# Kernel optimization log

Hardware: AMD Instinct MI355X
Metric: run time of the kernel (lower is better)

## Reference

```python
import jax, jax.numpy as jnp
import numpy as np

DIM_MODEL = 1024
NUM_HEADS = 16
HEAD_DIM = DIM_MODEL // NUM_HEADS


def setup_inputs() -> dict:
    key = jax.random.key(0)
    ks = jax.random.split(key, 10)
    B, S1, S2, D = 2, 1, 2048, DIM_MODEL
    q = jax.random.normal(ks[0], (B, S1, S2, 1, D), dtype=jnp.float32)
    k = jax.random.normal(ks[1], (B, S1, S2, 1, D), dtype=jnp.float32)
    v = jax.random.normal(ks[2], (B, S1, S2, 1, D), dtype=jnp.float32)
    mask = jnp.zeros((1,), dtype=jnp.bool_)
    inv_scale_factor = jnp.ones((1, 1, 1, 1), dtype=jnp.float32)
    s = 1.0 / np.sqrt(D)
    Wq = jax.random.uniform(ks[3], (D, D), jnp.float32, -s, s)
    bq = jax.random.uniform(ks[4], (D,), jnp.float32, -s, s)
    Wk = jax.random.uniform(ks[5], (D, D), jnp.float32, -s, s)
    bk = jax.random.uniform(ks[6], (D,), jnp.float32, -s, s)
    Wv = jax.random.uniform(ks[7], (D, D), jnp.float32, -s, s)
    bv = jax.random.uniform(ks[8], (D,), jnp.float32, -s, s)
    return {"q": q, "k": k, "v": v, "mask": mask, "inv_scale_factor": inv_scale_factor,
            "Wq": Wq, "bq": bq, "Wk": Wk, "bk": bk, "Wv": Wv, "bv": bv}


def reference(q, k, v, mask, inv_scale_factor, Wq, bq, Wk, bk, Wv, bv):
    # q,k,v: [B, S1, S2, 1, D]; mask is unused (faithful to source forward)
    B, S1, S2, _, D = q.shape
    H, Dh = NUM_HEADS, HEAD_DIM

    def proj(x, W, b):
        # torch Linear: x @ W.T + b, then view -> heads, transpose(2,3)
        y = jnp.einsum('bgsod,ed->bgsoe', x, W) + b  # o==1 collapses in reshape
        return jnp.swapaxes(y.reshape(B, S1, S2, H, Dh), 2, 3)  # [B,S1,H,S2,Dh]

    qh = proj(q, Wq, bq) / jnp.sqrt(jnp.asarray(Dh, q.dtype))
    kh = proj(k, Wk, bk)
    vh = proj(v, Wv, bv)

    scores = jnp.einsum('bghsd,bghtd->bghst', qh, kh) / inv_scale_factor  # [B,S1,H,S2,S2]
    p = jax.nn.softmax(scores.astype(jnp.float32), axis=-1).astype(q.dtype)
    # dropout_p=0 (eval): identity
    out = jnp.einsum('bghst,bghtd->bghsd', p, vh)  # [B,S1,H,S2,Dh]
    out = out.reshape(B, S1, H, S2 * Dh)
    out = jnp.transpose(out, (0, 1, 3, 2))  # torch transpose(2,3)
    return out.reshape(B, S1, -1)
```

## Files before the change

### kernel.cpp

```cpp
#include <hip/hip_runtime.h>
#include <stdint.h>

typedef short bf16x8 __attribute__((ext_vector_type(8)));
typedef float f32x4 __attribute__((ext_vector_type(4)));

static __device__ __forceinline__ unsigned short f2bf(float f) {
  union { float f; uint32_t u; } c; c.f = f;
  uint32_t u = c.u;
  uint32_t r = (u + 0x7fffu + ((u >> 16) & 1u)) >> 16;
  return (unsigned short)r;
}

extern "C" __device__ float __ocml_exp2_f32(float);
static __device__ __forceinline__ float exp2_(float x) {
#if __has_builtin(__builtin_amdgcn_exp2f)
  return __builtin_amdgcn_exp2f(x);
#else
  return __ocml_exp2_f32(x);
#endif
}

static __device__ __forceinline__ uint32_t cvtpk_bf16(float a, float b) {
  uint32_t r;
  asm("v_cvt_pk_bf16_f32 %0, %1, %2" : "=v"(r) : "v"(a), "v"(b));
  return r;
}

__device__ __forceinline__ void gload_lds16(const void* g, void* l) {
  __builtin_amdgcn_global_load_lds((const __attribute__((address_space(1))) uint32_t*)g,
                                   (__attribute__((address_space(3))) uint32_t*)l, 16, 0, 0);
}

__global__ __launch_bounds__(256) void k_convert(
    const float* __restrict__ q, const float* __restrict__ k, const float* __restrict__ v,
    const float* __restrict__ Wq, const float* __restrict__ Wk, const float* __restrict__ Wv,
    unsigned short* __restrict__ Xb, unsigned short* __restrict__ Wb) {
  const int NX4 = 3145728;
  const int NW4 = 786432;
  int i = blockIdx.x * 256 + threadIdx.x;
  if (i >= NX4 + NW4) return;
  const float* src; unsigned short* dst; int off4;
  if (i < NX4) {
    int a = i >> 20; off4 = i & 1048575;
    src = (a == 0) ? q : (a == 1) ? k : v;
    dst = Xb + (size_t)a * 4194304;
  } else {
    int j = i - NX4;
    int a = j >> 18; off4 = j & 262143;
    src = (a == 0) ? Wq : (a == 1) ? Wk : Wv;
    dst = Wb + (size_t)a * 1048576;
  }
  float4 f = ((const float4*)src)[off4];
  uint32_t lo = (uint32_t)f2bf(f.x) | ((uint32_t)f2bf(f.y) << 16);
  uint32_t hi = (uint32_t)f2bf(f.z) | ((uint32_t)f2bf(f.w) << 16);
  ((uint2*)dst)[off4] = make_uint2(lo, hi);
}

__global__ __launch_bounds__(256) void k_proj(
    const unsigned short* __restrict__ Xb, const unsigned short* __restrict__ Wb,
    const float* __restrict__ bq, const float* __restrict__ bk, const float* __restrict__ bv,
    const float* __restrict__ inv_scale,
    unsigned short* __restrict__ Qh, unsigned short* __restrict__ Kh,
    unsigned short* __restrict__ VhT) {
  __shared__ __align__(16) unsigned short At[128 * 32];
  __shared__ __align__(16) unsigned short Bt[128 * 32];
  const int g = blockIdx.y;
  const int m0 = (blockIdx.x & 31) * 128, n0 = (blockIdx.x >> 5) * 128;
  const unsigned short* X = Xb + (size_t)g * 4194304;
  const unsigned short* W = Wb + (size_t)g * 1048576;
  const int tid = threadIdx.x;
  const int w = tid >> 6, lane = tid & 63;
  const int wr = w >> 1, wc = w & 1;
  const int lq = lane & 15, lg = lane >> 4;

  f32x4 acc[4][4];
#pragma unroll
  for (int a = 0; a < 4; a++)
#pragma unroll
    for (int b = 0; b < 4; b++) acc[a][b] = (f32x4){0.f, 0.f, 0.f, 0.f};

  for (int kt = 0; kt < 32; ++kt) {
#pragma unroll
    for (int p = 0; p < 2; ++p) {
      int i = (w * 2 + p) * 64 + lane;
      int row = i >> 2, c = i & 3;
      gload_lds16(X + (size_t)(m0 + row) * 1024 + kt * 32 + c * 8, (char*)At + i * 16);
      gload_lds16(W + (size_t)(n0 + row) * 1024 + kt * 32 + c * 8, (char*)Bt + i * 16);
    }
    __syncthreads();
    bf16x8 af[4], bfr[4];
#pragma unroll
    for (int mi = 0; mi < 4; mi++)
      af[mi] = *(const bf16x8*)((const char*)At + ((wr * 64 + mi * 16 + lq) * 64 + lg * 16));
#pragma unroll
    for (int ni = 0; ni < 4; ni++)
      bfr[ni] = *(const bf16x8*)((const char*)Bt + ((wc * 64 + ni * 16 + lq) * 64 + lg * 16));
#pragma unroll
    for (int mi = 0; mi < 4; mi++)
#pragma unroll
      for (int ni = 0; ni < 4; ni++)
        acc[mi][ni] = __builtin_amdgcn_mfma_f32_16x16x32_bf16(af[mi], bfr[ni], acc[mi][ni], 0, 0, 0);
    __syncthreads();
  }

  const float* bias = (g == 0) ? bq : (g == 1) ? bk : bv;
  const float scale = (g == 0) ? 0.125f * 1.4426950408889634f / inv_scale[0] : 1.0f;
#pragma unroll
  for (int ni = 0; ni < 4; ni++) {
    int col = n0 + wc * 64 + ni * 16 + lq;
    float bb = bias[col];
    int h = col >> 6, dh = col & 63;
#pragma unroll
    for (int mi = 0; mi < 4; mi++) {
#pragma unroll
      for (int r = 0; r < 4; r++) {
        int row = m0 + wr * 64 + mi * 16 + lg * 4 + r;
        int b = row >> 11, s2 = row & 2047;
        unsigned short bv16 = f2bf((acc[mi][ni][r] + bb) * scale);
        if (g == 0)
          Qh[(size_t)(b * 16 + h) * 131072 + (size_t)s2 * 64 + dh] = bv16;
        else if (g == 1)
          Kh[(size_t)(b * 16 + h) * 131072 + (size_t)s2 * 64 + dh] = bv16;
        else
          VhT[(size_t)((b * 16 + h) * 64 + dh) * 2048 + s2] = bv16;
      }
    }
  }
}

__global__ __launch_bounds__(256, 2) void k_attn(
    const unsigned short* __restrict__ Qh, const unsigned short* __restrict__ Kh,
    const unsigned short* __restrict__ VhT, float* __restrict__ Ot) {
  __shared__ __align__(16) unsigned short Kt[3][64 * 64];
  __shared__ __align__(16) unsigned short Vt[3][64 * 64];
  __shared__ __align__(16) unsigned short Pl[4][32][64];
  const int n = blockIdx.x;
  const int xcd = n & 7, slot = n >> 3;
  const int bh = (xcd << 2) | (slot >> 4);
  const int qt = slot & 15;
  const int tid = threadIdx.x;
  const int w = tid >> 6, lane = tid & 63;
  const int lq = lane & 15, lg = lane >> 4;
  const int qbase = qt * 128 + w * 32;

  bf16x8 qf[2][2];
#pragma unroll
  for (int r = 0; r < 2; r++) {
    const unsigned short* qp = Qh + ((size_t)bh * 2048 + qbase + r * 16 + lq) * 64 + lg * 8;
    qf[r][0] = *(const bf16x8*)(qp);
    qf[r][1] = *(const bf16x8*)(qp + 32);
  }

  f32x4 ofr[4][2];
#pragma unroll
  for (int dt = 0; dt < 4; dt++)
#pragma unroll
    for (int r = 0; r < 2; r++) ofr[dt][r] = (f32x4){0.f, 0.f, 0.f, 0.f};
  float m[2] = {-INFINITY, -INFINITY}, l[2] = {0.f, 0.f};

  const unsigned short* kgbase = Kh + (size_t)bh * 131072;
  const unsigned short* vgbase = VhT + (size_t)bh * 131072;

  auto STAGE = [&](int tile, int buf) {
#pragma unroll
    for (int p = 0; p < 2; ++p) {
      int i = p * 256 + tid;
      int row = i >> 3, c = i & 7;
      int cs = c ^ (row & 7);
      gload_lds16(kgbase + (size_t)(tile * 64 + row) * 64 + cs * 8, (char*)Kt[buf] + i * 16);
      gload_lds16(vgbase + (size_t)row * 2048 + tile * 64 + cs * 8, (char*)Vt[buf] + i * 16);
    }
  };

  STAGE(0, 0);
  STAGE(1, 1);

  for (int kv = 0; kv < 32; ++kv) {
    if (kv == 31) {
      asm volatile("s_waitcnt vmcnt(0)" ::: "memory");
    } else {
      asm volatile("s_waitcnt vmcnt(4)" ::: "memory");
    }
    __builtin_amdgcn_s_barrier();
    __builtin_amdgcn_sched_barrier(0);

    if (kv < 30) STAGE(kv + 2, (kv + 2) % 3);

    const char* ktc = (const char*)Kt[kv % 3];
    const char* vtc = (const char*)Vt[kv % 3];

    f32x4 sf[4][2];
#pragma unroll
    for (int t4 = 0; t4 < 4; t4++) {
      int row = t4 * 16 + lq;
      int c0 = lg ^ (row & 7), c1 = (4 + lg) ^ (row & 7);
      bf16x8 ka = *(const bf16x8*)(ktc + row * 128 + c0 * 16);
      bf16x8 kc = *(const bf16x8*)(ktc + row * 128 + c1 * 16);
#pragma unroll
      for (int r = 0; r < 2; r++) {
        f32x4 z = (f32x4){0.f, 0.f, 0.f, 0.f};
        z = __builtin_amdgcn_mfma_f32_16x16x32_bf16(ka, qf[r][0], z, 0, 0, 0);
        z = __builtin_amdgcn_mfma_f32_16x16x32_bf16(kc, qf[r][1], z, 0, 0, 0);
        sf[t4][r] = z;
      }
    }

    float pmax[2];
#pragma unroll
    for (int r = 0; r < 2; r++) {
      float a0 = fmaxf(fmaxf(sf[0][r][0], sf[0][r][1]), fmaxf(sf[0][r][2], sf[0][r][3]));
      float a1 = fmaxf(fmaxf(sf[1][r][0], sf[1][r][1]), fmaxf(sf[1][r][2], sf[1][r][3]));
      float a2 = fmaxf(fmaxf(sf[2][r][0], sf[2][r][1]), fmaxf(sf[2][r][2], sf[2][r][3]));
      float a3 = fmaxf(fmaxf(sf[3][r][0], sf[3][r][1]), fmaxf(sf[3][r][2], sf[3][r][3]));
      float a = fmaxf(fmaxf(a0, a1), fmaxf(a2, a3));
      a = fmaxf(a, __shfl_xor(a, 16));
      a = fmaxf(a, __shfl_xor(a, 32));
      pmax[r] = a;
    }
    if (__any((pmax[0] > m[0] + 8.f) || (pmax[1] > m[1] + 8.f))) {
#pragma unroll
      for (int r = 0; r < 2; r++) {
        float mn = fmaxf(m[r], pmax[r]);
        float c = exp2_(m[r] - mn);
        m[r] = mn;
        l[r] *= c;
#pragma unroll
        for (int dt = 0; dt < 4; dt++) ofr[dt][r] *= c;
      }
    }

#pragma unroll
    for (int r = 0; r < 2; r++) {
      float ps = 0.f;
#pragma unroll
      for (int t4 = 0; t4 < 4; t4++) {
        float p0 = exp2_(sf[t4][r][0] - m[r]);
        float p1 = exp2_(sf[t4][r][1] - m[r]);
        float p2 = exp2_(sf[t4][r][2] - m[r]);
        float p3 = exp2_(sf[t4][r][3] - m[r]);
        ps += (p0 + p1) + (p2 + p3);
        uint32_t w0 = cvtpk_bf16(p0, p1);
        uint32_t w1 = cvtpk_bf16(p2, p3);
        uint64_t dw = (uint64_t)w0 | ((uint64_t)w1 << 32);
        int ch = (t4 * 2 + (lg >> 1)) ^ (lq & 7);
        __builtin_memcpy((char*)&Pl[w][r * 16 + lq][0] + ch * 16 + (lg & 1) * 8, &dw, 8);
      }
      ps += __shfl_xor(ps, 16);
      ps += __shfl_xor(ps, 32);
      l[r] += ps;
    }

    bf16x8 pf[2][2];
#pragma unroll
    for (int r = 0; r < 2; r++)
#pragma unroll
      for (int c = 0; c < 2; c++) {
        int ch = (c * 4 + lg) ^ (lq & 7);
        __builtin_memcpy(&pf[r][c], (const char*)&Pl[w][r * 16 + lq][0] + ch * 16, 16);
      }
    __builtin_amdgcn_s_setprio(1);
#pragma unroll
    for (int dt = 0; dt < 4; dt++) {
      int row = dt * 16 + lq;
      int c0 = lg ^ (row & 7), c1 = (4 + lg) ^ (row & 7);
      bf16x8 va = *(const bf16x8*)(vtc + row * 128 + c0 * 16);
      bf16x8 vc = *(const bf16x8*)(vtc + row * 128 + c1 * 16);
#pragma unroll
      for (int r = 0; r < 2; r++) {
        ofr[dt][r] = __builtin_amdgcn_mfma_f32_16x16x32_bf16(va, pf[r][0], ofr[dt][r], 0, 0, 0);
        ofr[dt][r] = __builtin_amdgcn_mfma_f32_16x16x32_bf16(vc, pf[r][1], ofr[dt][r], 0, 0, 0);
      }
    }
    __builtin_amdgcn_s_setprio(0);
  }

  float rl[2] = {1.0f / l[0], 1.0f / l[1]};
#pragma unroll
  for (int dt = 0; dt < 4; dt++)
#pragma unroll
    for (int r = 0; r < 2; r++) {
      f32x4 o = ofr[dt][r] * rl[r];
      size_t q = qbase + r * 16 + lq;
      *(f32x4*)(Ot + ((size_t)bh * 2048 + q) * 64 + dt * 16 + lg * 4) = o;
    }
}

__global__ __launch_bounds__(256) void k_tr(const float* __restrict__ Ot,
                                            float* __restrict__ out) {
  int u = blockIdx.x * 256 + threadIdx.x;
  int h4 = u & 3, dh = (u >> 2) & 63, s2 = (u >> 8) & 2047, b = u >> 19;
  size_t base = ((size_t)(b * 16 + h4 * 4) * 2048 + s2) * 64 + dh;
  float4 o;
  o.x = Ot[base];
  o.y = Ot[base + 131072];
  o.z = Ot[base + 262144];
  o.w = Ot[base + 393216];
  ((float4*)out)[u] = o;
}

extern "C" void kernel_launch(void* const* d_in, const int* in_sizes, int n_in,
                              void* d_out, int out_size, void* d_ws, size_t ws_size,
                              hipStream_t stream) {
  const float* q   = (const float*)d_in[0];
  const float* k   = (const float*)d_in[1];
  const float* v   = (const float*)d_in[2];
  const float* inv = (const float*)d_in[4];
  const float* Wq  = (const float*)d_in[5];
  const float* bq  = (const float*)d_in[6];
  const float* Wk  = (const float*)d_in[7];
  const float* bk  = (const float*)d_in[8];
  const float* Wv  = (const float*)d_in[9];
  const float* bv  = (const float*)d_in[10];

  char* ws = (char*)d_ws;
  unsigned short* Xb  = (unsigned short*)(ws);
  unsigned short* Wb  = (unsigned short*)(ws + 25165824);
  unsigned short* Qh  = (unsigned short*)(ws + 31457280);
  unsigned short* Kh  = (unsigned short*)(ws + 39845888);
  unsigned short* VhT = (unsigned short*)(ws + 48234496);
  float*          Ot  = (float*)(ws);

  k_convert<<<15360, 256, 0, stream>>>(q, k, v, Wq, Wk, Wv, Xb, Wb);
  k_proj<<<dim3(256, 3), 256, 0, stream>>>(Xb, Wb, bq, bk, bv, inv, Qh, Kh, VhT);
  k_attn<<<512, 256, 0, stream>>>(Qh, Kh, VhT, Ot);
  k_tr<<<4096, 256, 0, stream>>>(Ot, (float*)d_out);
}
```

Before: 125.3 us.

## Triple-buffer projection GEMM loads and store attention output in bf16

```diff
diff --git a/kernel.cpp b/kernel.cpp
--- a/kernel.cpp
+++ b/kernel.cpp
@@ -9,6 +9,11 @@
   uint32_t u = c.u;
   uint32_t r = (u + 0x7fffu + ((u >> 16) & 1u)) >> 16;
   return (unsigned short)r;
+}
+
+static __device__ __forceinline__ float bf2f(unsigned short s) {
+  union { uint32_t u; float f; } c; c.u = ((uint32_t)s) << 16;
+  return c.f;
 }
 
 extern "C" __device__ float __ocml_exp2_f32(float);
@@ -62,8 +67,8 @@
     const float* __restrict__ inv_scale,
     unsigned short* __restrict__ Qh, unsigned short* __restrict__ Kh,
     unsigned short* __restrict__ VhT) {
-  __shared__ __align__(16) unsigned short At[128 * 32];
-  __shared__ __align__(16) unsigned short Bt[128 * 32];
+  __shared__ __align__(16) unsigned short At[3][128 * 32];
+  __shared__ __align__(16) unsigned short Bt[3][128 * 32];
   const int g = blockIdx.y;
   const int m0 = (blockIdx.x & 31) * 128, n0 = (blockIdx.x >> 5) * 128;
   const unsigned short* X = Xb + (size_t)g * 4194304;
@@ -79,28 +84,44 @@
 #pragma unroll
     for (int b = 0; b < 4; b++) acc[a][b] = (f32x4){0.f, 0.f, 0.f, 0.f};
 
-  for (int kt = 0; kt < 32; ++kt) {
+  auto STAGE = [&](int kt, int buf) {
 #pragma unroll
     for (int p = 0; p < 2; ++p) {
       int i = (w * 2 + p) * 64 + lane;
       int row = i >> 2, c = i & 3;
-      gload_lds16(X + (size_t)(m0 + row) * 1024 + kt * 32 + c * 8, (char*)At + i * 16);
-      gload_lds16(W + (size_t)(n0 + row) * 1024 + kt * 32 + c * 8, (char*)Bt + i * 16);
-    }
-    __syncthreads();
+      gload_lds16(X + (size_t)(m0 + row) * 1024 + kt * 32 + c * 8, (char*)At[buf] + i * 16);
+      gload_lds16(W + (size_t)(n0 + row) * 1024 + kt * 32 + c * 8, (char*)Bt[buf] + i * 16);
+    }
+  };
+
+  STAGE(0, 0);
+  STAGE(1, 1);
+
+  for (int kt = 0; kt < 32; ++kt) {
+    if (kt == 31) {
+      asm volatile("s_waitcnt vmcnt(0)" ::: "memory");
+    } else {
+      asm volatile("s_waitcnt vmcnt(4)" ::: "memory");
+    }
+    __builtin_amdgcn_s_barrier();
+    __builtin_amdgcn_sched_barrier(0);
+
+    if (kt < 30) STAGE(kt + 2, (kt + 2) % 3);
+
+    const char* at = (const char*)At[kt % 3];
+    const char* bt = (const char*)Bt[kt % 3];
     bf16x8 af[4], bfr[4];
 #pragma unroll
     for (int mi = 0; mi < 4; mi++)
-      af[mi] = *(const bf16x8*)((const char*)At + ((wr * 64 + mi * 16 + lq) * 64 + lg * 16));
+      af[mi] = *(const bf16x8*)(at + ((wr * 64 + mi * 16 + lq) * 64 + lg * 16));
 #pragma unroll
     for (int ni = 0; ni < 4; ni++)
-      bfr[ni] = *(const bf16x8*)((const char*)Bt + ((wc * 64 + ni * 16 + lq) * 64 + lg * 16));
+      bfr[ni] = *(const bf16x8*)(bt + ((wc * 64 + ni * 16 + lq) * 64 + lg * 16));
 #pragma unroll
     for (int mi = 0; mi < 4; mi++)
 #pragma unroll
       for (int ni = 0; ni < 4; ni++)
         acc[mi][ni] = __builtin_amdgcn_mfma_f32_16x16x32_bf16(af[mi], bfr[ni], acc[mi][ni], 0, 0, 0);
-    __syncthreads();
   }
 
   const float* bias = (g == 0) ? bq : (g == 1) ? bk : bv;
@@ -130,7 +151,7 @@
 
 __global__ __launch_bounds__(256, 2) void k_attn(
     const unsigned short* __restrict__ Qh, const unsigned short* __restrict__ Kh,
-    const unsigned short* __restrict__ VhT, float* __restrict__ Ot) {
+    const unsigned short* __restrict__ VhT, unsigned short* __restrict__ Ot) {
   __shared__ __align__(16) unsigned short Kt[3][64 * 64];
   __shared__ __align__(16) unsigned short Vt[3][64 * 64];
   __shared__ __align__(16) unsigned short Pl[4][32][64];
@@ -280,21 +301,22 @@
 #pragma unroll
     for (int r = 0; r < 2; r++) {
       f32x4 o = ofr[dt][r] * rl[r];
+      uint2 pk = make_uint2(cvtpk_bf16(o[0], o[1]), cvtpk_bf16(o[2], o[3]));
       size_t q = qbase + r * 16 + lq;
-      *(f32x4*)(Ot + ((size_t)bh * 2048 + q) * 64 + dt * 16 + lg * 4) = o;
-    }
-}
-
-__global__ __launch_bounds__(256) void k_tr(const float* __restrict__ Ot,
+      *(uint2*)(Ot + ((size_t)bh * 2048 + q) * 64 + dt * 16 + lg * 4) = pk;
+    }
+}
+
+__global__ __launch_bounds__(256) void k_tr(const unsigned short* __restrict__ Ot,
                                             float* __restrict__ out) {
   int u = blockIdx.x * 256 + threadIdx.x;
   int h4 = u & 3, dh = (u >> 2) & 63, s2 = (u >> 8) & 2047, b = u >> 19;
   size_t base = ((size_t)(b * 16 + h4 * 4) * 2048 + s2) * 64 + dh;
   float4 o;
-  o.x = Ot[base];
-  o.y = Ot[base + 131072];
-  o.z = Ot[base + 262144];
-  o.w = Ot[base + 393216];
+  o.x = bf2f(Ot[base]);
+  o.y = bf2f(Ot[base + 131072]);
+  o.z = bf2f(Ot[base + 262144]);
+  o.w = bf2f(Ot[base + 393216]);
   ((float4*)out)[u] = o;
 }
 
@@ -318,7 +340,7 @@
   unsigned short* Qh  = (unsigned short*)(ws + 31457280);
   unsigned short* Kh  = (unsigned short*)(ws + 39845888);
   unsigned short* VhT = (unsigned short*)(ws + 48234496);
-  float*          Ot  = (float*)(ws);
+  unsigned short* Ot  = (unsigned short*)(ws);
 
   k_convert<<<15360, 256, 0, stream>>>(q, k, v, Wq, Wk, Wv, Xb, Wb);
   k_proj<<<dim3(256, 3), 256, 0, stream>>>(Xb, Wb, bq, bk, bv, inv, Qh, Kh, VhT);
```

New measurement: 124.5 us, median of 2. Within noise of the previous version (-0.7%).
